# Optimization experiments

Measured on AMD Instinct MI355X. Metric: run time of the kernel, lower is better.

The kernel has to match this reference:

```python
import jax, jax.numpy as jnp
import numpy as np

# Config matching init_kwargs / module defaults
B_T2I, B_LM, B_MMU = 2, 2, 2
B = B_T2I + B_LM + B_MMU
S = 1280
H, D = 16, 64
IMAGE_BE = [(128, 1152)]          # t2i_image_begin_end
MMU_END = 1027
PAD_BE = [(0, 80), (0, 100), (0, 110), (0, 0)]  # create_block_mask default pad_begin_ends


def _mixed_mask():
    """Vectorized translation of OmniAttentionMechanism.mixed_mask -> bool [B,S,S]."""
    q = jnp.arange(S)[:, None]    # [S,1] query index
    kv = jnp.arange(S)[None, :]   # [1,S] key index

    # t2i_full_begin / t2i_full_end (per-q image block bounds)
    full_begin = jnp.arange(S)
    full_end = jnp.arange(S)
    for ib, ie in IMAGE_BE:
        full_begin = full_begin.at[ib:ie].set(ib)
        full_end = full_end.at[ib:ie].set(ie)

    # pad_ends[b, kv]: arange baseline, first len(PAD_BE) batches get pad region end
    pad_ends = jnp.tile(jnp.arange(S)[None, :], (B, 1))
    for cnt, (pb, pe) in enumerate(PAD_BE):
        pad_ends = pad_ends.at[cnt, pb:pe].set(pe)

    # t2i: padded-causal OR bidirectional image block
    causal = (~(kv < pad_ends[:, None, :]) & (q >= kv)) | (q == kv)   # [B,S,S]
    full = (kv < full_end[:, None]) & (kv >= full_begin[:, None])     # [S,S] (q-indexed bounds)
    t2i = causal | full[None]
    lm = (q >= kv)[None]                                              # [1,S,S]
    mmu = ((q >= kv) | (kv < MMU_END))[None]                          # [1,S,S]

    b = jnp.arange(B)[:, None, None]
    # Faithful to the original XOR composition (terms are batch-disjoint so == OR)
    return ((b < B_T2I) & t2i) ^ ((b >= B_T2I) & (b < B_T2I + B_LM) & lm) ^ ((b >= B_T2I + B_LM) & mmu)


def setup_inputs() -> dict:
    key = jax.random.key(0)
    kq, kk, kv = jax.random.split(key, 3)
    shape = (B, H, S, D)
    return {
        "q": jax.random.normal(kq, shape, dtype=jnp.float32),
        "k": jax.random.normal(kk, shape, dtype=jnp.float32),
        "v": jax.random.normal(kv, shape, dtype=jnp.float32),
    }


def reference(q, k, v):
    """flex_attention(q, k, v, block_mask=mixed-t2i-lm-mmu) equivalent."""
    mask = _mixed_mask()[:, None]  # [B,1,S,S], broadcast over heads
    scale = 1.0 / jnp.sqrt(jnp.float32(D))  # flex_attention default scale
    scores = jnp.einsum('bhqd,bhkd->bhqk', q, k) * scale
    scores = jnp.where(mask, scores, -jnp.inf)  # every row has >=1 allowed key (q==kv / q>=kv)
    attn = jax.nn.softmax(scores, axis=-1)
    return jnp.einsum('bhqk,bhkd->bhqd', attn, v)
```

## Files before the change

### kernel.cpp

```cpp
#include <hip/hip_runtime.h>
#include <hip/hip_bf16.h>
#include <math.h>


#define SS 1280
#define DD 64
#define NH 16
#define TK 64
#define QB 128

typedef __attribute__((ext_vector_type(8))) short bf16x8;
typedef __attribute__((ext_vector_type(16))) float f32x16;

union UA { uint u[4]; bf16x8 v; };

__device__ inline uint pk2(float a, float b) {
    union { __hip_bfloat162 h; uint u; } cv;
    cv.h = __float22bfloat162_rn(float2{a, b});
    return cv.u;
}

__device__ inline void pl32(uint& a, uint& b) {
    asm volatile("v_permlane32_swap_b32 %0, %1" : "+v"(a), "+v"(b));
}

__global__ __launch_bounds__(256) void prepass8(
    const float* __restrict__ K, const float* __restrict__ V,
    ushort* __restrict__ Kb, ushort* __restrict__ Vtb)
{
    const int gx = blockIdx.x;
    const int t  = threadIdx.x;
    if (gx < 3840) {
        const size_t e = ((size_t)gx * 256 + t) * 8;
        const float4 a = *(const float4*)(K + e);
        const float4 c = *(const float4*)(K + e + 4);
        UA u;
        u.u[0] = pk2(a.x, a.y); u.u[1] = pk2(a.z, a.w);
        u.u[2] = pk2(c.x, c.y); u.u[3] = pk2(c.z, c.w);
        *(bf16x8*)(Kb + e) = u.v;
    } else {
        const int g   = gx - 3840;
        const int kvt = g % 20;
        const int p   = g / 20;
        __shared__ float T[64 * 67];
        const float* src = V + (size_t)p * (SS * DD) + (size_t)(kvt * 64) * DD;
#pragma unroll
        for (int i = 0; i < 16; ++i) {
            const int idx = t + 256 * i;
            T[(idx >> 6) * 67 + (idx & 63)] = src[idx];
        }
        __syncthreads();
        ushort* dst = Vtb + (size_t)p * (DD * SS) + kvt * 64;
#pragma unroll
        for (int i = 0; i < 2; ++i) {
            const int c0 = t + 256 * i;
            const int d = c0 >> 3, kc = c0 & 7;
            UA u;
#pragma unroll
            for (int j = 0; j < 4; ++j)
                u.u[j] = pk2(T[(kc * 8 + 2 * j) * 67 + d], T[(kc * 8 + 2 * j + 1) * 67 + d]);
            *(bf16x8*)(dst + (size_t)d * SS + kc * 8) = u.v;
        }
    }
}

__global__ __launch_bounds__(256) void omni_attn9(
    const float* __restrict__ Q, const ushort* __restrict__ Kb,
    const ushort* __restrict__ Vtb, float* __restrict__ O)
{
    const int bid = blockIdx.x;
    const int x   = bid & 7;
    const int j   = bid >> 3;
    const int qt  = j % 10;
    const int p   = (j / 10) * 8 + x;
    const int b   = p >> 4;
    const int h   = p & 15;

    const int t   = threadIdx.x;
    const int w   = t >> 6;
    const int l   = t & 63;
    const int l31 = l & 31;
    const int hi2 = l >> 5;

    const int qb0 = qt * QB;
    const int qw0 = qb0 + w * 32;
    const int qr  = qw0 + l31;
    const size_t pbase = (size_t)p * (SS * DD);

    const int bt = (b < 2) ? 0 : (b < 4) ? 1 : 2;
    const int pe = (b == 0) ? 80 : (b == 1) ? 100 : 0;
    const int qmax_blk = qb0 + QB - 1;
    const int qmax_w   = qw0 + 31;
    const bool blk_img = (qb0 + QB - 1 >= 128) && (qb0 < 1152);
    const bool w_img   = (qw0 >= 128) && (qw0 < 1152);

    __shared__ char smem[32768];

    bf16x8 qf[4];
#pragma unroll
    for (int ks = 0; ks < 4; ++ks) {
        const float* src = Q + pbase + (size_t)qr * DD + ks * 16 + hi2 * 8;
        const float4 a = *(const float4*)(src);
        const float4 c = *(const float4*)(src + 4);
        UA u;
        u.u[0] = pk2(a.x, a.y); u.u[1] = pk2(a.z, a.w);
        u.u[2] = pk2(c.x, c.y); u.u[3] = pk2(c.z, c.w);
        qf[ks] = u.v;
    }

    const float scale = 0.125f * 1.44269504088896340736f;

    f32x16 o_acc[2];
#pragma unroll
    for (int ntd = 0; ntd < 2; ++ntd)
#pragma unroll
        for (int r = 0; r < 16; ++r) o_acc[ntd][r] = 0.f;
    float psum = 0.f;

    auto need_blk = [&](int k0) -> bool {
        if (bt == 0) return (k0 <= qmax_blk) || (blk_img && k0 >= 128 && k0 < 1152);
        if (bt == 1) return (k0 <= qmax_blk);
        return (k0 <= qmax_blk) || (k0 < 1027);
    };
    auto next_tile = [&](int k) -> int {
        k += TK;
        while (k < SS && !need_blk(k)) k += TK;
        return k;
    };

    int koff[2], voff[2];
#pragma unroll
    for (int rd = 0; rd < 2; ++rd) {
        const int ci  = rd * 256 + w * 64 + l;
        const int row = ci >> 3, cc = ci & 7;
        koff[rd] = row * DD + (cc ^ (row & 7)) * 8;
        const int d = ci >> 3, vc = ci & 7;
        voff[rd] = d * SS + (vc ^ ((d ^ (d >> 3)) & 7)) * 8;
    }

    auto stage = [&](int bsel, int k0) {
        char* buf = smem + bsel * 16384;
        const ushort* Kp = Kb + pbase + (size_t)k0 * DD;
        const ushort* Vp = Vtb + pbase + k0;
#pragma unroll
        for (int rd = 0; rd < 2; ++rd) {
            char* lb = buf + (rd * 256 + w * 64) * 16;
            __builtin_amdgcn_global_load_lds(
                (const __attribute__((address_space(1))) void*)(Kp + koff[rd]),
                (__attribute__((address_space(3))) void*)lb, 16, 0, 0);
        }
#pragma unroll
        for (int rd = 0; rd < 2; ++rd) {
            char* lb = buf + 8192 + (rd * 256 + w * 64) * 16;
            __builtin_amdgcn_global_load_lds(
                (const __attribute__((address_space(1))) void*)(Vp + voff[rd]),
                (__attribute__((address_space(3))) void*)lb, 16, 0, 0);
        }
    };

    int k0 = 0, cur = 0;
    int k1 = next_tile(0);
    stage(0, 0);
    __syncthreads();

    while (true) {
        if (k1 < SS) stage(cur ^ 1, k1);

        char* cbuf = smem + cur * 16384;
        const bool kv_img = (k0 >= 128) && (k0 < 1152);
        bool need_w, full_w;
        if (bt == 0) {
            need_w = (k0 <= qmax_w) || (w_img && kv_img);
            full_w = ((k0 >= pe) && (k0 + 63 <= qw0)) || (w_img && kv_img);
        } else if (bt == 1) {
            need_w = (k0 <= qmax_w);
            full_w = (k0 + 63 <= qw0);
        } else {
            need_w = (k0 <= qmax_w) || (k0 < 1027);
            full_w = (k0 + 63 <= qw0) || (k0 + 63 < 1027);
        }

        if (need_w) {
#pragma unroll
            for (int nt = 0; nt < 2; ++nt) {
                f32x16 s;
#pragma unroll
                for (int r = 0; r < 16; ++r) s[r] = 0.f;
                __builtin_amdgcn_s_setprio(1);
#pragma unroll
                for (int ksd = 0; ksd < 4; ++ksd) {
                    const int row = nt * 32 + l31;
                    int off = row * 128 + ksd * 32 + hi2 * 16;
                    off ^= (row & 7) << 4;
                    const bf16x8 kf = *(const bf16x8*)(cbuf + off);
                    s = __builtin_amdgcn_mfma_f32_32x32x16_bf16(kf, qf[ksd], s, 0, 0, 0);
                }
                __builtin_amdgcn_s_setprio(0);

                const int c0 = k0 + nt * 32;
                uint c[8];
#pragma unroll
                for (int i = 0; i < 8; ++i) {
                    float pa, pb;
                    if (full_w) {
                        pa = exp2f(s[2 * i] * scale);
                        pb = exp2f(s[2 * i + 1] * scale);
                    } else {
                        const int r0i = 2 * i, r1i = 2 * i + 1;
                        const int kva = c0 + (r0i & 3) + 8 * (r0i >> 2) + 4 * hi2;
                        const int kvb = c0 + (r1i & 3) + 8 * (r1i >> 2) + 4 * hi2;
                        bool aa, ab;
                        if (bt == 0) {
                            aa = (qr == kva) | ((kva >= pe) & (qr >= kva)) |
                                 ((qr >= 128) & (qr < 1152) & (kva >= 128) & (kva < 1152));
                            ab = (qr == kvb) | ((kvb >= pe) & (qr >= kvb)) |
                                 ((qr >= 128) & (qr < 1152) & (kvb >= 128) & (kvb < 1152));
                        } else if (bt == 1) {
                            aa = (qr >= kva); ab = (qr >= kvb);
                        } else {
                            aa = (qr >= kva) | (kva < 1027);
                            ab = (qr >= kvb) | (kvb < 1027);
                        }
                        pa = aa ? exp2f(s[2 * i] * scale) : 0.f;
                        pb = ab ? exp2f(s[2 * i + 1] * scale) : 0.f;
                    }
                    psum += pa + pb;
                    c[i] = pk2(pa, pb);
                }

                UA A0, A1;
                {
                    uint a0 = c[0], b0 = c[2]; pl32(a0, b0);
                    uint a1 = c[1], b1 = c[3]; pl32(a1, b1);
                    A0.u[0] = a0; A0.u[1] = a1; A0.u[2] = b0; A0.u[3] = b1;
                    uint a2 = c[4], b2 = c[6]; pl32(a2, b2);
                    uint a3 = c[5], b3 = c[7]; pl32(a3, b3);
                    A1.u[0] = a2; A1.u[1] = a3; A1.u[2] = b2; A1.u[3] = b3;
                }

                __builtin_amdgcn_s_setprio(1);
#pragma unroll
                for (int ntd = 0; ntd < 2; ++ntd) {
                    const int row = ntd * 32 + l31;
                    const int swz = ((row ^ (row >> 3)) & 7) << 4;
                    int off0 = 8192 + row * 128 + (2 * nt) * 32 + hi2 * 16;     off0 ^= swz;
                    int off1 = 8192 + row * 128 + (2 * nt + 1) * 32 + hi2 * 16; off1 ^= swz;
                    const bf16x8 vf0 = *(const bf16x8*)(cbuf + off0);
                    o_acc[ntd] = __builtin_amdgcn_mfma_f32_32x32x16_bf16(A0.v, vf0, o_acc[ntd], 0, 0, 0);
                    const bf16x8 vf1 = *(const bf16x8*)(cbuf + off1);
                    o_acc[ntd] = __builtin_amdgcn_mfma_f32_32x32x16_bf16(A1.v, vf1, o_acc[ntd], 0, 0, 0);
                }
                __builtin_amdgcn_s_setprio(0);
            }
        }

        __syncthreads();
        if (k1 >= SS) break;
        k0 = k1; k1 = next_tile(k1); cur ^= 1;
    }

    psum += __shfl_xor(psum, 32, 64);
#pragma unroll
    for (int r = 0; r < 16; ++r) {
        const int q_loc = (r & 3) + 8 * (r >> 2) + 4 * hi2;
        const float tv = __shfl(psum, q_loc, 64);
        const float iv = 1.f / tv;
        float* dst = O + pbase + (size_t)(qw0 + q_loc) * DD + l31;
#pragma unroll
        for (int ntd = 0; ntd < 2; ++ntd)
            dst[ntd * 32] = o_acc[ntd][r] * iv;
    }
}

extern "C" void kernel_launch(void* const* d_in, const int* in_sizes, int n_in,
                              void* d_out, int out_size, void* d_ws, size_t ws_size,
                              hipStream_t stream) {
    const float* q = (const float*)d_in[0];
    const float* k = (const float*)d_in[1];
    const float* v = (const float*)d_in[2];
    float* o = (float*)d_out;

    const size_t NE = 7864320ULL;
    ushort* Kb  = (ushort*)d_ws;
    ushort* Vtb = Kb + NE;

    prepass8<<<dim3(5760), 256, 0, stream>>>(k, v, Kb, Vtb);
    omni_attn9<<<dim3(960), 256, 0, stream>>>(q, Kb, Vtb, o);
}
```

Before: 120.7 us.

## Use persistent workgroups with atomic work queue ordered longest-first

Replaces the static one-block-per-tile grid with 640 persistent workgroups that pull (batch, head, q-tile) items from a global atomic counter. Items are decoded in an order that puts the heaviest tiles (full-image and late causal tiles) first, so uneven per-tile work under the mixed mask is balanced. It adds a counter-reset kernel launch, an atomic plus barrier per item, and Q load and setup repeated inside the loop.

```diff
diff --git a/kernel.cpp b/kernel.cpp
--- a/kernel.cpp
+++ b/kernel.cpp
@@ -8,6 +8,7 @@
 #define NH 16
 #define TK 64
 #define QB 128
+#define NITEMS 960
 
 typedef __attribute__((ext_vector_type(8))) short bf16x8;
 typedef __attribute__((ext_vector_type(16))) float f32x16;
@@ -23,6 +24,26 @@
 __device__ inline void pl32(uint& a, uint& b) {
     asm volatile("v_permlane32_swap_b32 %0, %1" : "+v"(a), "+v"(b));
 }
+
+__device__ inline void decode_item(int i, int& b, int& h, int& qt) {
+    if (i < 96)  { qt = 9; b = i / 16; h = i % 16; return; }
+    i -= 96;
+    if (i < 256) { b = i / 128; qt = 1 + (i % 128) / 16; h = i % 16; return; }
+    i -= 256;
+    if (i < 32)  { b = 2 + i / 16; qt = 8; h = i % 16; return; }
+    i -= 32;
+    if (i < 32)  { b = 4 + i / 16; qt = 8; h = i % 16; return; }
+    i -= 32;
+    if (i < 256) { b = 4 + i / 128; qt = (i % 128) / 16; h = i % 16; return; }
+    i -= 256;
+    if (i < 224) { qt = 7 - i / 32; b = 2 + (i % 32) / 16; h = i % 16; return; }
+    i -= 224;
+    if (i < 32)  { b = 2 + i / 16; qt = 0; h = i % 16; return; }
+    i -= 32;
+    b = i / 16; qt = 0; h = i % 16;
+}
+
+__global__ void zero_ctr_kernel(int* ctr) { if (threadIdx.x == 0) *ctr = 0; }
 
 __global__ __launch_bounds__(256) void prepass8(
     const float* __restrict__ K, const float* __restrict__ V,
@@ -64,69 +85,20 @@
     }
 }
 
-__global__ __launch_bounds__(256) void omni_attn9(
+__global__ __launch_bounds__(256) void omni_attn11(
     const float* __restrict__ Q, const ushort* __restrict__ Kb,
-    const ushort* __restrict__ Vtb, float* __restrict__ O)
+    const ushort* __restrict__ Vtb, float* __restrict__ O, int* __restrict__ ctr)
 {
-    const int bid = blockIdx.x;
-    const int x   = bid & 7;
-    const int j   = bid >> 3;
-    const int qt  = j % 10;
-    const int p   = (j / 10) * 8 + x;
-    const int b   = p >> 4;
-    const int h   = p & 15;
-
     const int t   = threadIdx.x;
     const int w   = t >> 6;
     const int l   = t & 63;
     const int l31 = l & 31;
     const int hi2 = l >> 5;
 
-    const int qb0 = qt * QB;
-    const int qw0 = qb0 + w * 32;
-    const int qr  = qw0 + l31;
-    const size_t pbase = (size_t)p * (SS * DD);
-
-    const int bt = (b < 2) ? 0 : (b < 4) ? 1 : 2;
-    const int pe = (b == 0) ? 80 : (b == 1) ? 100 : 0;
-    const int qmax_blk = qb0 + QB - 1;
-    const int qmax_w   = qw0 + 31;
-    const bool blk_img = (qb0 + QB - 1 >= 128) && (qb0 < 1152);
-    const bool w_img   = (qw0 >= 128) && (qw0 < 1152);
-
     __shared__ char smem[32768];
-
-    bf16x8 qf[4];
-#pragma unroll
-    for (int ks = 0; ks < 4; ++ks) {
-        const float* src = Q + pbase + (size_t)qr * DD + ks * 16 + hi2 * 8;
-        const float4 a = *(const float4*)(src);
-        const float4 c = *(const float4*)(src + 4);
-        UA u;
-        u.u[0] = pk2(a.x, a.y); u.u[1] = pk2(a.z, a.w);
-        u.u[2] = pk2(c.x, c.y); u.u[3] = pk2(c.z, c.w);
-        qf[ks] = u.v;
-    }
+    __shared__ int s_item;
 
     const float scale = 0.125f * 1.44269504088896340736f;
-
-    f32x16 o_acc[2];
-#pragma unroll
-    for (int ntd = 0; ntd < 2; ++ntd)
-#pragma unroll
-        for (int r = 0; r < 16; ++r) o_acc[ntd][r] = 0.f;
-    float psum = 0.f;
-
-    auto need_blk = [&](int k0) -> bool {
-        if (bt == 0) return (k0 <= qmax_blk) || (blk_img && k0 >= 128 && k0 < 1152);
-        if (bt == 1) return (k0 <= qmax_blk);
-        return (k0 <= qmax_blk) || (k0 < 1027);
-    };
-    auto next_tile = [&](int k) -> int {
-        k += TK;
-        while (k < SS && !need_blk(k)) k += TK;
-        return k;
-    };
 
     int koff[2], voff[2];
 #pragma unroll
@@ -138,137 +110,189 @@
         voff[rd] = d * SS + (vc ^ ((d ^ (d >> 3)) & 7)) * 8;
     }
 
-    auto stage = [&](int bsel, int k0) {
-        char* buf = smem + bsel * 16384;
-        const ushort* Kp = Kb + pbase + (size_t)k0 * DD;
-        const ushort* Vp = Vtb + pbase + k0;
-#pragma unroll
-        for (int rd = 0; rd < 2; ++rd) {
-            char* lb = buf + (rd * 256 + w * 64) * 16;
-            __builtin_amdgcn_global_load_lds(
-                (const __attribute__((address_space(1))) void*)(Kp + koff[rd]),
-                (__attribute__((address_space(3))) void*)lb, 16, 0, 0);
-        }
-#pragma unroll
-        for (int rd = 0; rd < 2; ++rd) {
-            char* lb = buf + 8192 + (rd * 256 + w * 64) * 16;
-            __builtin_amdgcn_global_load_lds(
-                (const __attribute__((address_space(1))) void*)(Vp + voff[rd]),
-                (__attribute__((address_space(3))) void*)lb, 16, 0, 0);
-        }
-    };
-
-    int k0 = 0, cur = 0;
-    int k1 = next_tile(0);
-    stage(0, 0);
-    __syncthreads();
-
-    while (true) {
-        if (k1 < SS) stage(cur ^ 1, k1);
-
-        char* cbuf = smem + cur * 16384;
-        const bool kv_img = (k0 >= 128) && (k0 < 1152);
-        bool need_w, full_w;
-        if (bt == 0) {
-            need_w = (k0 <= qmax_w) || (w_img && kv_img);
-            full_w = ((k0 >= pe) && (k0 + 63 <= qw0)) || (w_img && kv_img);
-        } else if (bt == 1) {
-            need_w = (k0 <= qmax_w);
-            full_w = (k0 + 63 <= qw0);
-        } else {
-            need_w = (k0 <= qmax_w) || (k0 < 1027);
-            full_w = (k0 + 63 <= qw0) || (k0 + 63 < 1027);
-        }
-
-        if (need_w) {
-#pragma unroll
-            for (int nt = 0; nt < 2; ++nt) {
-                f32x16 s;
-#pragma unroll
-                for (int r = 0; r < 16; ++r) s[r] = 0.f;
-                __builtin_amdgcn_s_setprio(1);
-#pragma unroll
-                for (int ksd = 0; ksd < 4; ++ksd) {
-                    const int row = nt * 32 + l31;
-                    int off = row * 128 + ksd * 32 + hi2 * 16;
-                    off ^= (row & 7) << 4;
-                    const bf16x8 kf = *(const bf16x8*)(cbuf + off);
-                    s = __builtin_amdgcn_mfma_f32_32x32x16_bf16(kf, qf[ksd], s, 0, 0, 0);
+    for (;;) {
+        if (t == 0) s_item = atomicAdd(ctr, 1);
+        __syncthreads();
+        const int item = s_item;
+        if (item >= NITEMS) break;
+
+        int b, h, qt;
+        decode_item(item, b, h, qt);
+        const int p   = b * NH + h;
+        const int qb0 = qt * QB;
+        const int qw0 = qb0 + w * 32;
+        const int qr  = qw0 + l31;
+        const size_t pbase = (size_t)p * (SS * DD);
+
+        const int bt = (b < 2) ? 0 : (b < 4) ? 1 : 2;
+        const int pe = (b == 0) ? 80 : (b == 1) ? 100 : 0;
+        const int qmax_blk = qb0 + QB - 1;
+        const int qmax_w   = qw0 + 31;
+        const bool blk_img = (qb0 + QB - 1 >= 128) && (qb0 < 1152);
+        const bool w_img   = (qw0 >= 128) && (qw0 < 1152);
+
+        bf16x8 qf[4];
+#pragma unroll
+        for (int ks = 0; ks < 4; ++ks) {
+            const float* src = Q + pbase + (size_t)qr * DD + ks * 16 + hi2 * 8;
+            const float4 a = *(const float4*)(src);
+            const float4 c = *(const float4*)(src + 4);
+            UA u;
+            u.u[0] = pk2(a.x, a.y); u.u[1] = pk2(a.z, a.w);
+            u.u[2] = pk2(c.x, c.y); u.u[3] = pk2(c.z, c.w);
+            qf[ks] = u.v;
+        }
+
+        f32x16 o_acc[2];
+#pragma unroll
+        for (int ntd = 0; ntd < 2; ++ntd)
+#pragma unroll
+            for (int r = 0; r < 16; ++r) o_acc[ntd][r] = 0.f;
+        float psum = 0.f;
+
+        auto need_blk = [&](int k0) -> bool {
+            if (bt == 0) return (k0 <= qmax_blk) || (blk_img && k0 >= 128 && k0 < 1152);
+            if (bt == 1) return (k0 <= qmax_blk);
+            return (k0 <= qmax_blk) || (k0 < 1027);
+        };
+        auto next_tile = [&](int k) -> int {
+            k += TK;
+            while (k < SS && !need_blk(k)) k += TK;
+            return k;
+        };
+        auto stage = [&](int bsel, int k0) {
+            char* buf = smem + bsel * 16384;
+            const ushort* Kp = Kb + pbase + (size_t)k0 * DD;
+            const ushort* Vp = Vtb + pbase + k0;
+#pragma unroll
+            for (int rd = 0; rd < 2; ++rd) {
+                char* lb = buf + (rd * 256 + w * 64) * 16;
+                __builtin_amdgcn_global_load_lds(
+                    (const __attribute__((address_space(1))) void*)(Kp + koff[rd]),
+                    (__attribute__((address_space(3))) void*)lb, 16, 0, 0);
+            }
+#pragma unroll
+            for (int rd = 0; rd < 2; ++rd) {
+                char* lb = buf + 8192 + (rd * 256 + w * 64) * 16;
+                __builtin_amdgcn_global_load_lds(
+                    (const __attribute__((address_space(1))) void*)(Vp + voff[rd]),
+                    (__attribute__((address_space(3))) void*)lb, 16, 0, 0);
+            }
+        };
+
+        int k0 = 0, cur = 0;
+        int k1 = next_tile(0);
+        stage(0, 0);
+        __syncthreads();
+
+        while (true) {
+            if (k1 < SS) stage(cur ^ 1, k1);
+
+            char* cbuf = smem + cur * 16384;
+            const bool kv_img = (k0 >= 128) && (k0 < 1152);
+            bool need_w, full_w;
+            if (bt == 0) {
+                need_w = (k0 <= qmax_w) || (w_img && kv_img);
+                full_w = ((k0 >= pe) && (k0 + 63 <= qw0)) || (w_img && kv_img);
+            } else if (bt == 1) {
+                need_w = (k0 <= qmax_w);
+                full_w = (k0 + 63 <= qw0);
+            } else {
+                need_w = (k0 <= qmax_w) || (k0 < 1027);
+                full_w = (k0 + 63 <= qw0) || (k0 + 63 < 1027);
+            }
+
+            if (need_w) {
+#pragma unroll
+                for (int nt = 0; nt < 2; ++nt) {
+                    f32x16 s;
+#pragma unroll
+                    for (int r = 0; r < 16; ++r) s[r] = 0.f;
+                    __builtin_amdgcn_s_setprio(1);
+#pragma unroll
+                    for (int ksd = 0; ksd < 4; ++ksd) {
+                        const int row = nt * 32 + l31;
+                        int off = row * 128 + ksd * 32 + hi2 * 16;
+                        off ^= (row & 7) << 4;
+                        const bf16x8 kf = *(const bf16x8*)(cbuf + off);
+                        s = __builtin_amdgcn_mfma_f32_32x32x16_bf16(kf, qf[ksd], s, 0, 0, 0);
+                    }
+                    __builtin_amdgcn_s_setprio(0);
+
+                    const int c0 = k0 + nt * 32;
+                    uint c[8];
+#pragma unroll
+                    for (int i = 0; i < 8; ++i) {
+                        float pa, pb;
+                        if (full_w) {
+                            pa = exp2f(s[2 * i] * scale);
+                            pb = exp2f(s[2 * i + 1] * scale);
+                        } else {
+                            const int r0i = 2 * i, r1i = 2 * i + 1;
+                            const int kva = c0 + (r0i & 3) + 8 * (r0i >> 2) + 4 * hi2;
+                            const int kvb = c0 + (r1i & 3) + 8 * (r1i >> 2) + 4 * hi2;
+                            bool aa, ab;
+                            if (bt == 0) {
+                                aa = (qr == kva) | ((kva >= pe) & (qr >= kva)) |
+                                     ((qr >= 128) & (qr < 1152) & (kva >= 128) & (kva < 1152));
+                                ab = (qr == kvb) | ((kvb >= pe) & (qr >= kvb)) |
+                                     ((qr >= 128) & (qr < 1152) & (kvb >= 128) & (kvb < 1152));
+                            } else if (bt == 1) {
+                                aa = (qr >= kva); ab = (qr >= kvb);
+                            } else {
+                                aa = (qr >= kva) | (kva < 1027);
+                                ab = (qr >= kvb) | (kvb < 1027);
+                            }
+                            pa = aa ? exp2f(s[2 * i] * scale) : 0.f;
+                            pb = ab ? exp2f(s[2 * i + 1] * scale) : 0.f;
+                        }
+                        psum += pa + pb;
+                        c[i] = pk2(pa, pb);
+                    }
+
+                    UA A0, A1;
+                    {
+                        uint a0 = c[0], b0 = c[2]; pl32(a0, b0);
+                        uint a1 = c[1], b1 = c[3]; pl32(a1, b1);
+                        A0.u[0] = a0; A0.u[1] = a1; A0.u[2] = b0; A0.u[3] = b1;
+                        uint a2 = c[4], b2 = c[6]; pl32(a2, b2);
+                        uint a3 = c[5], b3 = c[7]; pl32(a3, b3);
+                        A1.u[0] = a2; A1.u[1] = a3; A1.u[2] = b2; A1.u[3] = b3;
+                    }
+
+                    __builtin_amdgcn_s_setprio(1);
+#pragma unroll
+                    for (int ntd = 0; ntd < 2; ++ntd) {
+                        const int row = ntd * 32 + l31;
+                        const int swz = ((row ^ (row >> 3)) & 7) << 4;
+                        int off0 = 8192 + row * 128 + (2 * nt) * 32 + hi2 * 16;     off0 ^= swz;
+                        int off1 = 8192 + row * 128 + (2 * nt + 1) * 32 + hi2 * 16; off1 ^= swz;
+                        const bf16x8 vf0 = *(const bf16x8*)(cbuf + off0);
+                        o_acc[ntd] = __builtin_amdgcn_mfma_f32_32x32x16_bf16(A0.v, vf0, o_acc[ntd], 0, 0, 0);
+                        const bf16x8 vf1 = *(const bf16x8*)(cbuf + off1);
+                        o_acc[ntd] = __builtin_amdgcn_mfma_f32_32x32x16_bf16(A1.v, vf1, o_acc[ntd], 0, 0, 0);
+                    }
+                    __builtin_amdgcn_s_setprio(0);
                 }
-                __builtin_amdgcn_s_setprio(0);
-
-                const int c0 = k0 + nt * 32;
-                uint c[8];
-#pragma unroll
-                for (int i = 0; i < 8; ++i) {
-                    float pa, pb;
-                    if (full_w) {
-                        pa = exp2f(s[2 * i] * scale);
-                        pb = exp2f(s[2 * i + 1] * scale);
-                    } else {
-                        const int r0i = 2 * i, r1i = 2 * i + 1;
-                        const int kva = c0 + (r0i & 3) + 8 * (r0i >> 2) + 4 * hi2;
-                        const int kvb = c0 + (r1i & 3) + 8 * (r1i >> 2) + 4 * hi2;
-                        bool aa, ab;
-                        if (bt == 0) {
-                            aa = (qr == kva) | ((kva >= pe) & (qr >= kva)) |
-                                 ((qr >= 128) & (qr < 1152) & (kva >= 128) & (kva < 1152));
-                            ab = (qr == kvb) | ((kvb >= pe) & (qr >= kvb)) |
-                                 ((qr >= 128) & (qr < 1152) & (kvb >= 128) & (kvb < 1152));
-                        } else if (bt == 1) {
-                            aa = (qr >= kva); ab = (qr >= kvb);
-                        } else {
-                            aa = (qr >= kva) | (kva < 1027);
-                            ab = (qr >= kvb) | (kvb < 1027);
-                        }
-                        pa = aa ? exp2f(s[2 * i] * scale) : 0.f;
-                        pb = ab ? exp2f(s[2 * i + 1] * scale) : 0.f;
-                    }
-                    psum += pa + pb;
-                    c[i] = pk2(pa, pb);
-                }
-
-                UA A0, A1;
-                {
-                    uint a0 = c[0], b0 = c[2]; pl32(a0, b0);
-                    uint a1 = c[1], b1 = c[3]; pl32(a1, b1);
-                    A0.u[0] = a0; A0.u[1] = a1; A0.u[2] = b0; A0.u[3] = b1;
-                    uint a2 = c[4], b2 = c[6]; pl32(a2, b2);
-                    uint a3 = c[5], b3 = c[7]; pl32(a3, b3);
-                    A1.u[0] = a2; A1.u[1] = a3; A1.u[2] = b2; A1.u[3] = b3;
-                }
-
-                __builtin_amdgcn_s_setprio(1);
-#pragma unroll
-                for (int ntd = 0; ntd < 2; ++ntd) {
-                    const int row = ntd * 32 + l31;
-                    const int swz = ((row ^ (row >> 3)) & 7) << 4;
-                    int off0 = 8192 + row * 128 + (2 * nt) * 32 + hi2 * 16;     off0 ^= swz;
-                    int off1 = 8192 + row * 128 + (2 * nt + 1) * 32 + hi2 * 16; off1 ^= swz;
-                    const bf16x8 vf0 = *(const bf16x8*)(cbuf + off0);
-                    o_acc[ntd] = __builtin_amdgcn_mfma_f32_32x32x16_bf16(A0.v, vf0, o_acc[ntd], 0, 0, 0);
-                    const bf16x8 vf1 = *(const bf16x8*)(cbuf + off1);
-                    o_acc[ntd] = __builtin_amdgcn_mfma_f32_32x32x16_bf16(A1.v, vf1, o_acc[ntd], 0, 0, 0);
-                }
-                __builtin_amdgcn_s_setprio(0);
             }
-        }
-
+
+            __syncthreads();
+            if (k1 >= SS) break;
+            k0 = k1; k1 = next_tile(k1); cur ^= 1;
+        }
+
+        psum += __shfl_xor(psum, 32, 64);
+#pragma unroll
+        for (int r = 0; r < 16; ++r) {
+            const int q_loc = (r & 3) + 8 * (r >> 2) + 4 * hi2;
+            const float tv = __shfl(psum, q_loc, 64);
+            const float iv = 1.f / tv;
+            float* dst = O + pbase + (size_t)(qw0 + q_loc) * DD + l31;
+#pragma unroll
+            for (int ntd = 0; ntd < 2; ++ntd)
+                dst[ntd * 32] = o_acc[ntd][r] * iv;
+        }
         __syncthreads();
-        if (k1 >= SS) break;
-        k0 = k1; k1 = next_tile(k1); cur ^= 1;
-    }
-
-    psum += __shfl_xor(psum, 32, 64);
-#pragma unroll
-    for (int r = 0; r < 16; ++r) {
-        const int q_loc = (r & 3) + 8 * (r >> 2) + 4 * hi2;
-        const float tv = __shfl(psum, q_loc, 64);
-        const float iv = 1.f / tv;
-        float* dst = O + pbase + (size_t)(qw0 + q_loc) * DD + l31;
-#pragma unroll
-        for (int ntd = 0; ntd < 2; ++ntd)
-            dst[ntd * 32] = o_acc[ntd][r] * iv;
     }
 }
 
@@ -283,7 +307,9 @@
     const size_t NE = 7864320ULL;
     ushort* Kb  = (ushort*)d_ws;
     ushort* Vtb = Kb + NE;
-
+    int* ctr    = (int*)((char*)d_ws + 2 * NE * sizeof(ushort));
+
+    zero_ctr_kernel<<<1, 64, 0, stream>>>(ctr);
     prepass8<<<dim3(5760), 256, 0, stream>>>(k, v, Kb, Vtb);
-    omni_attn9<<<dim3(960), 256, 0, stream>>>(q, Kb, Vtb, o);
-}
+    omni_attn11<<<dim3(640), 256, 0, stream>>>(q, Kb, Vtb, o, ctr);
+}
```

New measurement: 126.2 us. 1.05x slower.
